# Optimization experiments

Hardware: AMD Instinct MI355X
Metric: run time of the kernel (lower is better)

Reference implementation:

```python
import jax, jax.numpy as jnp
import numpy as np

D_STATE = 8
HIDDEN = 256


def _neighbor_sum(x):
    # frozen depthwise 3x3 conv, all-ones kernel with zero center, padding=1
    B, C, H, W = x.shape
    xp = jnp.pad(x, ((0, 0), (0, 0), (1, 1), (1, 1)))
    full = sum(xp[:, :, di:di + H, dj:dj + W] for di in range(3) for dj in range(3))
    return full - x  # subtract center tap


def setup_inputs() -> dict:
    key = jax.random.key(0)
    ks = jax.random.split(key, 6)
    B, H, W = 4, 256, 256
    c_in = 2 * D_STATE          # 16
    c_nbr = c_in * 8            # 128
    c_out = 8 * D_STATE         # 64
    s = 0.05
    return {
        "x_cat": jax.random.normal(ks[0], (B, c_in, H, W), dtype=jnp.float32),
        "w1": jax.random.normal(ks[1], (HIDDEN, c_nbr), dtype=jnp.float32) * s,
        "w2": jax.random.normal(ks[2], (HIDDEN, HIDDEN), dtype=jnp.float32) * s,
        "w3": jax.random.normal(ks[3], (HIDDEN, HIDDEN), dtype=jnp.float32) * s,
        "w4": jax.random.normal(ks[4], (HIDDEN, HIDDEN), dtype=jnp.float32) * s,
        "w5": jax.random.normal(ks[5], (c_out, HIDDEN), dtype=jnp.float32) * s,
    }


def reference(x_cat, w1, w2, w3, w4, w5):
    B, C, H, W = x_cat.shape
    d_state = C // 2
    # depthwise stencil: each of the 8 out-channels per group is the same neighbor sum
    nbr = _neighbor_sum(x_cat)                      # [B, 2d, H, W]
    xn = jnp.repeat(nbr, 8, axis=1)                 # [B, 16d, H, W]
    # five 1x1 convs with interleaved ELU (per-pixel MLP)
    h = jax.nn.elu(jnp.einsum('bchw,oc->bohw', xn, w1))
    h = jax.nn.elu(jnp.einsum('bchw,oc->bohw', h, w2))
    h = jax.nn.elu(jnp.einsum('bchw,oc->bohw', h, w3))
    h = jax.nn.elu(jnp.einsum('bchw,oc->bohw', h, w4))
    F_int = jnp.einsum('bchw,oc->bohw', h, w5)      # [B, 8d, H, W]
    d4 = 4 * d_state
    real = F_int[:, :d4].reshape(B, 4, d_state, H, W).mean(axis=1) * 0.1
    imag = F_int[:, d4:].reshape(B, 4, d_state, H, W).mean(axis=1) * 0.1
    return jnp.concatenate([real, imag], axis=1)    # [B, 2d, H, W]
```

## Files before the change

kernel.cpp:

```cpp
#include <hip/hip_runtime.h>

typedef __attribute__((ext_vector_type(8))) short bf16x8;
typedef __attribute__((ext_vector_type(4))) float f32x4;

__device__ __forceinline__ unsigned int f2bf(float f) {
  unsigned int u = __builtin_bit_cast(unsigned int, f);
  return (u + 0x7FFFu + ((u >> 16) & 1u)) >> 16;
}
__device__ __forceinline__ float eluf(float x) {
  return x > 0.f ? x : (__expf(x) - 1.f);
}
__device__ __forceinline__ unsigned int cvt_pk_bf16(float a, float b) {
  unsigned int r;
  asm("v_cvt_pk_bf16_f32 %0, %1, %2" : "=v"(r) : "v"(a), "v"(b));
  return r;
}

__global__ __launch_bounds__(256) void prep_kernel(
    const float* __restrict__ w1, const float* __restrict__ w2,
    const float* __restrict__ w3, const float* __restrict__ w4,
    const float* __restrict__ w5, unsigned short* __restrict__ ws) {
  int idx = blockIdx.x * 256 + threadIdx.x;
  float v = 0.f;
  if (idx < 8192) {
    int mt = idx >> 9, l = (idx >> 3) & 63, j = idx & 7;
    int o = mt * 16 + (l & 15), c = (l >> 4) * 8 + j;
    if (c < 16) {
      const float* r = w1 + o * 128 + c * 8;
      v = ((r[0] + r[1]) + (r[2] + r[3])) + ((r[4] + r[5]) + (r[6] + r[7]));
    }
  } else if (idx < 204800) {
    int t = idx - 8192;
    int which = t >> 16, e = t & 65535;
    const float* w = (which == 0) ? w2 : (which == 1) ? w3 : w4;
    int mt = e >> 12, kt = (e >> 9) & 7, l = (e >> 3) & 63, j = e & 7;
    int o = mt * 16 + (l & 15), c = kt * 32 + (l >> 4) * 8 + j;
    v = w[o * 256 + c];
  } else {
    int e = idx - 204800;
    int kt = e >> 9, l = (e >> 3) & 63, j = e & 7;
    int d = l & 15, c = kt * 32 + (l >> 4) * 8 + j;
    float s = 0.f;
    if (d < 8) {
      for (int g = 0; g < 4; ++g) s += w5[(g * 8 + d) * 256 + c];
    } else {
      for (int g = 0; g < 4; ++g) s += w5[(32 + g * 8 + (d - 8)) * 256 + c];
    }
    v = 0.025f * s;
  }
  ws[idx] = (unsigned short)f2bf(v);
}

#define ACT0 33792

__global__ __launch_bounds__(256, 3) void qca_kernel(
    const float* __restrict__ xcat, const unsigned short* __restrict__ wsu,
    float* __restrict__ out) {
  __shared__ __align__(16) char lds[38912];
  float* xt = reinterpret_cast<float*>(lds);

  const int tid = threadIdx.x;
  const int w = tid >> 6, l = tid & 63;
  const int l15 = l & 15, lhi = l >> 4;

  const int tile = blockIdx.x << 6;
  const int bimg = tile >> 16;
  const int y = (tile >> 8) & 255;
  const int x0 = tile & 255;

  for (int t = tid; t < 16 * 3 * 66; t += 256) {
    int c = t / 198;
    int rem = t - c * 198;
    int rr = rem / 66;
    int xl = rem - rr * 66;
    int gy = y + rr - 1, gx = x0 + xl - 1;
    float v = 0.f;
    if (gy >= 0 && gy < 256 && gx >= 0 && gx < 256)
      v = xcat[(size_t)(bimg * 16 + c) * 65536 + gy * 256 + gx];
    xt[t] = v;
  }
  __syncthreads();

  for (int t = tid; t < 2048; t += 256) {
    int p = t & 63, c = t >> 6;
    float v = 0.f;
    if (c < 16) {
      const float* bp = xt + c * 198 + (p + 1);
      v = (bp[-1] + bp[0] + bp[1]) + (bp[65] + bp[67]) +
          (bp[131] + bp[132] + bp[133]);
    }
    reinterpret_cast<unsigned short*>(lds + ACT0)[p * 40 + c] =
        (unsigned short)f2bf(v);
  }
  __syncthreads();

  const int lb_r = l15 * 528 + lhi * 16;
  const int lb_w = l15 * 528 + w * 128 + lhi * 8;
  const int lb_a1 = l15 * 80 + lhi * 16;

  f32x4 acc[4][4];

  auto epi = [&]() {
#pragma unroll
    for (int mi = 0; mi < 4; ++mi)
#pragma unroll
      for (int ni = 0; ni < 4; ++ni) {
        f32x4 v = acc[mi][ni];
        unsigned int u01 = cvt_pk_bf16(eluf(v[0]), eluf(v[1]));
        unsigned int u23 = cvt_pk_bf16(eluf(v[2]), eluf(v[3]));
        *reinterpret_cast<uint2*>(lds + lb_w + (ni * 8448 + mi * 32)) =
            uint2{u01, u23};
      }
  };

  {
#pragma unroll
    for (int mi = 0; mi < 4; ++mi)
#pragma unroll
      for (int ni = 0; ni < 4; ++ni) acc[mi][ni] = f32x4{0.f, 0.f, 0.f, 0.f};
    const bf16x8* w1v = reinterpret_cast<const bf16x8*>(wsu);
    bf16x8 bq[4];
#pragma unroll
    for (int ni = 0; ni < 4; ++ni)
      bq[ni] = *reinterpret_cast<const bf16x8*>(lds + ACT0 + lb_a1 + ni * 1280);
#pragma unroll
    for (int mi = 0; mi < 4; ++mi) {
      bf16x8 a = w1v[((w << 2) + mi) * 64 + l];
#pragma unroll
      for (int ni = 0; ni < 4; ++ni)
        acc[mi][ni] = __builtin_amdgcn_mfma_f32_16x16x32_bf16(
            a, bq[ni], acc[mi][ni], 0, 0, 0);
    }
    epi();
    __syncthreads();
  }

  auto mid = [&](const unsigned short* wbase) {
    const bf16x8* wv = reinterpret_cast<const bf16x8*>(wbase);
#pragma unroll
    for (int mi = 0; mi < 4; ++mi)
#pragma unroll
      for (int ni = 0; ni < 4; ++ni) acc[mi][ni] = f32x4{0.f, 0.f, 0.f, 0.f};
#pragma unroll
    for (int kt = 0; kt < 8; ++kt) {
      bf16x8 bq[4];
#pragma unroll
      for (int ni = 0; ni < 4; ++ni)
        bq[ni] = *reinterpret_cast<const bf16x8*>(
            lds + lb_r + (ni * 8448 + kt * 64));
#pragma unroll
      for (int mi = 0; mi < 4; ++mi) {
        bf16x8 a = wv[(((w << 2) + mi) * 8 + kt) * 64 + l];
#pragma unroll
        for (int ni = 0; ni < 4; ++ni)
          acc[mi][ni] = __builtin_amdgcn_mfma_f32_16x16x32_bf16(
              a, bq[ni], acc[mi][ni], 0, 0, 0);
      }
    }
    __syncthreads();
    epi();
    __syncthreads();
  };

  mid(wsu + 8192);
  mid(wsu + 73728);
  mid(wsu + 139264);

  {
    const bf16x8* w5v = reinterpret_cast<const bf16x8*>(wsu + 204800);
    f32x4 a5 = f32x4{0.f, 0.f, 0.f, 0.f};
    const int p = (w << 4) + l15;
    const int lb5 = p * 528 + lhi * 16;
#pragma unroll
    for (int kt = 0; kt < 8; ++kt) {
      bf16x8 a = w5v[kt * 64 + l];
      bf16x8 b = *reinterpret_cast<const bf16x8*>(lds + lb5 + kt * 64);
      a5 = __builtin_amdgcn_mfma_f32_16x16x32_bf16(a, b, a5, 0, 0, 0);
    }
    int pix = tile + p;
    int rem = pix & 65535;
    float* op = out + (size_t)(pix >> 16) * 1048576 + rem;
#pragma unroll
    for (int r = 0; r < 4; ++r) op[(lhi * 4 + r) * 65536] = a5[r];
  }
}

extern "C" void kernel_launch(void* const* d_in, const int* in_sizes, int n_in,
                              void* d_out, int out_size, void* d_ws,
                              size_t ws_size, hipStream_t stream) {
  const float* xcat = (const float*)d_in[0];
  const float* w1 = (const float*)d_in[1];
  const float* w2 = (const float*)d_in[2];
  const float* w3 = (const float*)d_in[3];
  const float* w4 = (const float*)d_in[4];
  const float* w5 = (const float*)d_in[5];
  unsigned short* ws = (unsigned short*)d_ws;
  float* out = (float*)d_out;

  prep_kernel<<<816, 256, 0, stream>>>(w1, w2, w3, w4, w5, ws);
  qca_kernel<<<4096, 256, 0, stream>>>(xcat, ws, out);
}
```

Measured before the change: 141.7 us.

## Switch to fp16 MFMA and compute ELU+1 with folded bias correction

Moves weights and activations from bf16 to fp16 and uses the f16 MFMA variant. The ELU epilogue is rewritten as a branchless max(z+1, exp(min(z,0))), which stores ELU(z)+1. The resulting constant offset is cancelled by precomputed per-output bias terms (minus the row sums of the next layer's weights), injected as the MFMA accumulator initial value. This removes the compare/select and per-element subtraction from the epilogue. It also drops the explicit zero-initialisation of the accumulators. In exchange, the prep kernel has to run serial 256-element reductions, and fp16 range and precision replace bf16.

New measurement: 203.1 us. 43.3% more time.

```diff
diff --git a/kernel.cpp b/kernel.cpp
--- a/kernel.cpp
+++ b/kernel.cpp
@@ -1,19 +1,19 @@
 #include <hip/hip_runtime.h>
 
-typedef __attribute__((ext_vector_type(8))) short bf16x8;
+typedef __attribute__((ext_vector_type(8))) _Float16 f16x8;
+typedef __attribute__((ext_vector_type(2))) __fp16 fp16x2;
 typedef __attribute__((ext_vector_type(4))) float f32x4;
 
-__device__ __forceinline__ unsigned int f2bf(float f) {
-  unsigned int u = __builtin_bit_cast(unsigned int, f);
-  return (u + 0x7FFFu + ((u >> 16) & 1u)) >> 16;
-}
-__device__ __forceinline__ float eluf(float x) {
-  return x > 0.f ? x : (__expf(x) - 1.f);
-}
-__device__ __forceinline__ unsigned int cvt_pk_bf16(float a, float b) {
-  unsigned int r;
-  asm("v_cvt_pk_bf16_f32 %0, %1, %2" : "=v"(r) : "v"(a), "v"(b));
-  return r;
+__device__ __forceinline__ unsigned short f2h(float f) {
+  _Float16 h = (_Float16)f;
+  return __builtin_bit_cast(unsigned short, h);
+}
+
+__device__ __forceinline__ unsigned int elu1_pk(float z0, float z1) {
+  float g0 = fmaxf(z0 + 1.f, __expf(fminf(z0, 0.f)));
+  float g1 = fmaxf(z1 + 1.f, __expf(fminf(z1, 0.f)));
+  fp16x2 p = __builtin_amdgcn_cvt_pkrtz(g0, g1);
+  return __builtin_bit_cast(unsigned int, p);
 }
 
 __global__ __launch_bounds__(256) void prep_kernel(
@@ -21,6 +21,30 @@
     const float* __restrict__ w3, const float* __restrict__ w4,
     const float* __restrict__ w5, unsigned short* __restrict__ ws) {
   int idx = blockIdx.x * 256 + threadIdx.x;
+  if (idx >= 209680) return;
+  if (idx >= 208896) {
+    int t = idx - 208896;
+    float* fb = reinterpret_cast<float*>(ws + 208896);
+    float s = 0.f;
+    if (t < 768) {
+      int which = t >> 8, o = t & 255;
+      const float* wp = (which == 0) ? w2 : (which == 1) ? w3 : w4;
+      for (int c = 0; c < 256; ++c) s += (float)(_Float16)wp[o * 256 + c];
+    } else {
+      int d = t - 768;
+      for (int c = 0; c < 256; ++c) {
+        float v = 0.f;
+        if (d < 8) {
+          for (int g = 0; g < 4; ++g) v += w5[(g * 8 + d) * 256 + c];
+        } else {
+          for (int g = 0; g < 4; ++g) v += w5[(32 + g * 8 + (d - 8)) * 256 + c];
+        }
+        s += (float)(_Float16)(0.025f * v);
+      }
+    }
+    fb[t] = -s;
+    return;
+  }
   float v = 0.f;
   if (idx < 8192) {
     int mt = idx >> 9, l = (idx >> 3) & 63, j = idx & 7;
@@ -32,10 +56,10 @@
   } else if (idx < 204800) {
     int t = idx - 8192;
     int which = t >> 16, e = t & 65535;
-    const float* w = (which == 0) ? w2 : (which == 1) ? w3 : w4;
+    const float* wp = (which == 0) ? w2 : (which == 1) ? w3 : w4;
     int mt = e >> 12, kt = (e >> 9) & 7, l = (e >> 3) & 63, j = e & 7;
     int o = mt * 16 + (l & 15), c = kt * 32 + (l >> 4) * 8 + j;
-    v = w[o * 256 + c];
+    v = wp[o * 256 + c];
   } else {
     int e = idx - 204800;
     int kt = e >> 9, l = (e >> 3) & 63, j = e & 7;
@@ -48,7 +72,7 @@
     }
     v = 0.025f * s;
   }
-  ws[idx] = (unsigned short)f2bf(v);
+  ws[idx] = f2h(v);
 }
 
 #define ACT0 33792
@@ -67,6 +91,8 @@
   const int bimg = tile >> 16;
   const int y = (tile >> 8) & 255;
   const int x0 = tile & 255;
+
+  const float* bias = reinterpret_cast<const float*>(wsu + 208896);
 
   for (int t = tid; t < 16 * 3 * 66; t += 256) {
     int c = t / 198;
@@ -89,8 +115,7 @@
       v = (bp[-1] + bp[0] + bp[1]) + (bp[65] + bp[67]) +
           (bp[131] + bp[132] + bp[133]);
     }
-    reinterpret_cast<unsigned short*>(lds + ACT0)[p * 40 + c] =
-        (unsigned short)f2bf(v);
+    reinterpret_cast<unsigned short*>(lds + ACT0)[p * 40 + c] = f2h(v);
   }
   __syncthreads();
 
@@ -106,54 +131,62 @@
 #pragma unroll
       for (int ni = 0; ni < 4; ++ni) {
         f32x4 v = acc[mi][ni];
-        unsigned int u01 = cvt_pk_bf16(eluf(v[0]), eluf(v[1]));
-        unsigned int u23 = cvt_pk_bf16(eluf(v[2]), eluf(v[3]));
+        unsigned int u01 = elu1_pk(v[0], v[1]);
+        unsigned int u23 = elu1_pk(v[2], v[3]);
         *reinterpret_cast<uint2*>(lds + lb_w + (ni * 8448 + mi * 32)) =
             uint2{u01, u23};
       }
   };
 
   {
-#pragma unroll
-    for (int mi = 0; mi < 4; ++mi)
-#pragma unroll
-      for (int ni = 0; ni < 4; ++ni) acc[mi][ni] = f32x4{0.f, 0.f, 0.f, 0.f};
-    const bf16x8* w1v = reinterpret_cast<const bf16x8*>(wsu);
-    bf16x8 bq[4];
+    const f16x8* w1v = reinterpret_cast<const f16x8*>(wsu);
+    f16x8 bq[4];
 #pragma unroll
     for (int ni = 0; ni < 4; ++ni)
-      bq[ni] = *reinterpret_cast<const bf16x8*>(lds + ACT0 + lb_a1 + ni * 1280);
+      bq[ni] = *reinterpret_cast<const f16x8*>(lds + ACT0 + lb_a1 + ni * 1280);
 #pragma unroll
     for (int mi = 0; mi < 4; ++mi) {
-      bf16x8 a = w1v[((w << 2) + mi) * 64 + l];
+      f16x8 a = w1v[((w << 2) + mi) * 64 + l];
 #pragma unroll
       for (int ni = 0; ni < 4; ++ni)
-        acc[mi][ni] = __builtin_amdgcn_mfma_f32_16x16x32_bf16(
-            a, bq[ni], acc[mi][ni], 0, 0, 0);
+        acc[mi][ni] = __builtin_amdgcn_mfma_f32_16x16x32_f16(
+            a, bq[ni], f32x4{0.f, 0.f, 0.f, 0.f}, 0, 0, 0);
     }
     epi();
     __syncthreads();
   }
 
-  auto mid = [&](const unsigned short* wbase) {
-    const bf16x8* wv = reinterpret_cast<const bf16x8*>(wbase);
-#pragma unroll
-    for (int mi = 0; mi < 4; ++mi)
-#pragma unroll
-      for (int ni = 0; ni < 4; ++ni) acc[mi][ni] = f32x4{0.f, 0.f, 0.f, 0.f};
-#pragma unroll
-    for (int kt = 0; kt < 8; ++kt) {
-      bf16x8 bq[4];
+  auto mid = [&](const unsigned short* wbase, const float* bptr) {
+    const f16x8* wv = reinterpret_cast<const f16x8*>(wbase);
+    {
+      f16x8 bq[4];
 #pragma unroll
       for (int ni = 0; ni < 4; ++ni)
-        bq[ni] = *reinterpret_cast<const bf16x8*>(
+        bq[ni] = *reinterpret_cast<const f16x8*>(lds + lb_r + ni * 8448);
+#pragma unroll
+      for (int mi = 0; mi < 4; ++mi) {
+        f16x8 a = wv[(((w << 2) + mi) * 8) * 64 + l];
+        f32x4 bv =
+            *reinterpret_cast<const f32x4*>(bptr + w * 64 + mi * 16 + lhi * 4);
+#pragma unroll
+        for (int ni = 0; ni < 4; ++ni)
+          acc[mi][ni] =
+              __builtin_amdgcn_mfma_f32_16x16x32_f16(a, bq[ni], bv, 0, 0, 0);
+      }
+    }
+#pragma unroll
+    for (int kt = 1; kt < 8; ++kt) {
+      f16x8 bq[4];
+#pragma unroll
+      for (int ni = 0; ni < 4; ++ni)
+        bq[ni] = *reinterpret_cast<const f16x8*>(
             lds + lb_r + (ni * 8448 + kt * 64));
 #pragma unroll
       for (int mi = 0; mi < 4; ++mi) {
-        bf16x8 a = wv[(((w << 2) + mi) * 8 + kt) * 64 + l];
+        f16x8 a = wv[(((w << 2) + mi) * 8 + kt) * 64 + l];
 #pragma unroll
         for (int ni = 0; ni < 4; ++ni)
-          acc[mi][ni] = __builtin_amdgcn_mfma_f32_16x16x32_bf16(
+          acc[mi][ni] = __builtin_amdgcn_mfma_f32_16x16x32_f16(
               a, bq[ni], acc[mi][ni], 0, 0, 0);
       }
     }
@@ -162,20 +195,25 @@
     __syncthreads();
   };
 
-  mid(wsu + 8192);
-  mid(wsu + 73728);
-  mid(wsu + 139264);
+  mid(wsu + 8192, bias);
+  mid(wsu + 73728, bias + 256);
+  mid(wsu + 139264, bias + 512);
 
   {
-    const bf16x8* w5v = reinterpret_cast<const bf16x8*>(wsu + 204800);
-    f32x4 a5 = f32x4{0.f, 0.f, 0.f, 0.f};
+    const f16x8* w5v = reinterpret_cast<const f16x8*>(wsu + 204800);
     const int p = (w << 4) + l15;
     const int lb5 = p * 528 + lhi * 16;
-#pragma unroll
-    for (int kt = 0; kt < 8; ++kt) {
-      bf16x8 a = w5v[kt * 64 + l];
-      bf16x8 b = *reinterpret_cast<const bf16x8*>(lds + lb5 + kt * 64);
-      a5 = __builtin_amdgcn_mfma_f32_16x16x32_bf16(a, b, a5, 0, 0, 0);
+    f32x4 a5 = *reinterpret_cast<const f32x4*>(bias + 768 + lhi * 4);
+    {
+      f16x8 a = w5v[l];
+      f16x8 b = *reinterpret_cast<const f16x8*>(lds + lb5);
+      a5 = __builtin_amdgcn_mfma_f32_16x16x32_f16(a, b, a5, 0, 0, 0);
+    }
+#pragma unroll
+    for (int kt = 1; kt < 8; ++kt) {
+      f16x8 a = w5v[kt * 64 + l];
+      f16x8 b = *reinterpret_cast<const f16x8*>(lds + lb5 + kt * 64);
+      a5 = __builtin_amdgcn_mfma_f32_16x16x32_f16(a, b, a5, 0, 0, 0);
     }
     int pix = tile + p;
     int rem = pix & 65535;
@@ -197,6 +235,6 @@
   unsigned short* ws = (unsigned short*)d_ws;
   float* out = (float*)d_out;
 
-  prep_kernel<<<816, 256, 0, stream>>>(w1, w2, w3, w4, w5, ws);
+  prep_kernel<<<820, 256, 0, stream>>>(w1, w2, w3, w4, w5, ws);
   qca_kernel<<<4096, 256, 0, stream>>>(xcat, ws, out);
 }
```
